# Kernel tuning notes

Hardware: AMD Instinct MI355X
Metric: run time of the kernel (lower is better)

The kernel has to match this reference:

```python
import jax, jax.numpy as jnp
import numpy as np

EPS = 1e-6

def feature_map(x):
    # 'elu' feature map: elu(x) + 1 (positive feature map from Katharopoulos et al.)
    return jax.nn.elu(x) + 1.0

def setup_inputs() -> dict:
    key = jax.random.key(0)
    kq, kk, kv = jax.random.split(key, 3)
    B, L, H, D = 4, 2048, 16, 64
    q = jax.random.normal(kq, (B, L, H, D), dtype=jnp.float32)
    k = jax.random.normal(kk, (B, L, H, D), dtype=jnp.float32)
    v = jax.random.normal(kv, (B, L, H, D), dtype=jnp.float32)
    return {"q": q, "k": k, "v": v}

def reference(q, k, v):
    # q, k, v: [N, L, H, D]  (attention_mask=None -> causal linear attention)
    qf = feature_map(q)
    kf = feature_map(k)
    # normalizer: z[n,l,h] = sum_d qf[n,l,h,d] * cumsum_s<=l kf[n,s,h,d]
    z = jnp.einsum('nlhd,nlhd->nlh', qf, jnp.cumsum(kf, axis=1)) + EPS
    # causal_dot_product via scan over sequence with carry S[n,h,d,m]
    B, L, H, D = q.shape
    M = v.shape[-1]
    qs = jnp.moveaxis(qf, 1, 0)  # [L, N, H, D]
    ks = jnp.moveaxis(kf, 1, 0)
    vs = jnp.moveaxis(v, 1, 0)

    def step(S, qkv):
        ql, kl, vl = qkv                              # [N,H,D], [N,H,D], [N,H,M]
        S = S + jnp.einsum('nhd,nhm->nhdm', kl, vl)   # running sum of k v^T
        out = jnp.einsum('nhd,nhdm->nhm', ql, S)
        return S, out

    S0 = jnp.zeros((B, H, D, M), dtype=q.dtype)
    _, outs = jax.lax.scan(step, S0, (qs, ks, vs))    # outs: [L, N, H, M]
    v_ = jnp.moveaxis(outs, 0, 1)                     # [N, L, H, M]
    return v_ / z[..., None]
```

## Files before the change

kernel.cpp:

```cpp
#include <hip/hip_runtime.h>
#include <cstdint>

#define LL 2048
#define HH 16
#define DD 64
#define LSTR 1024
#define EPSF 1e-6f
#define PAD 72
#define SWZ(row, off) ((row)*PAD + ((off) ^ ((((row)>>3)&7)<<3)))

typedef __bf16 bf16x8 __attribute__((ext_vector_type(8)));
typedef float floatx4 __attribute__((ext_vector_type(4)));
typedef unsigned short ushortx8 __attribute__((ext_vector_type(8)));
typedef unsigned short ushortx4 __attribute__((ext_vector_type(4)));
typedef unsigned short ushortx2 __attribute__((ext_vector_type(2)));

static __device__ __forceinline__ float fmap(float x){ return x > 0.f ? x + 1.f : __expf(x); }
static __device__ __forceinline__ unsigned short f2bf(float f){
    unsigned u = __builtin_bit_cast(unsigned, f);
    u += 0x7fffu + ((u >> 16) & 1u);
    return (unsigned short)(u >> 16);
}
static __device__ __forceinline__ float bf2f(unsigned short s){
    unsigned u = ((unsigned)s) << 16;
    return __builtin_bit_cast(float, u);
}
static __device__ __forceinline__ bf16x8 ldf(const unsigned short* p){
    return __builtin_bit_cast(bf16x8, *(const ushortx8*)p);
}

template<bool MAP>
static __device__ __forceinline__ void st_sd(unsigned short* base, int r, int c, float4 a, float4 b){
    if (MAP) {
        *(ushortx4*)(base + r*PAD + c)     = ushortx4{ f2bf(fmap(a.x)), f2bf(fmap(a.y)), f2bf(fmap(a.z)), f2bf(fmap(a.w)) };
        *(ushortx4*)(base + (r+1)*PAD + c) = ushortx4{ f2bf(fmap(b.x)), f2bf(fmap(b.y)), f2bf(fmap(b.z)), f2bf(fmap(b.w)) };
    } else {
        *(ushortx4*)(base + r*PAD + c)     = ushortx4{ f2bf(a.x), f2bf(a.y), f2bf(a.z), f2bf(a.w) };
        *(ushortx4*)(base + (r+1)*PAD + c) = ushortx4{ f2bf(b.x), f2bf(b.y), f2bf(b.z), f2bf(b.w) };
    }
}
template<bool MAP>
static __device__ __forceinline__ void st_tr(unsigned short* base, int r, int c, float4 a, float4 b){
    float aa[4] = {a.x, a.y, a.z, a.w}, bb[4] = {b.x, b.y, b.z, b.w};
#pragma unroll
    for (int e = 0; e < 4; ++e) {
        float x0 = MAP ? fmap(aa[e]) : aa[e];
        float x1 = MAP ? fmap(bb[e]) : bb[e];
        *(ushortx2*)(base + SWZ(c+e, r)) = ushortx2{ f2bf(x0), f2bf(x1) };
    }
}

__global__ __launch_bounds__(256) void kA(const float* __restrict__ kp, const float* __restrict__ vp,
                                          unsigned short* __restrict__ snap, float* __restrict__ ksnap)
{
    __shared__ __align__(16) unsigned short kft[2][DD*PAD];
    __shared__ __align__(16) unsigned short vtt[2][DD*PAD];
    const int blk = blockIdx.x;
    const int bh = blk >> 3, oct = blk & 7, b = bh >> 4, h = bh & 15;
    const int t = threadIdx.x;
    const int w = t >> 6, lane = t & 63, quad = lane >> 4, lr = lane & 15;
    const int m0 = 16*w;

    floatx4 acc[4];
#pragma unroll
    for (int dt = 0; dt < 4; ++dt) acc[dt] = floatx4{0.f,0.f,0.f,0.f};
    float ksa = 0.f;

    const int64_t gb0 = ((int64_t)(b*LL + oct*256)*HH + h)*DD;
#pragma unroll
    for (int ii = 0; ii < 2; ++ii) {
        int flat = t + 256*ii;
        int l0s = (flat >> 4) * 2, col4 = (flat & 15) << 2;
        const float* gk = kp + gb0 + (int64_t)l0s*LSTR + col4;
        const float* gv = vp + gb0 + (int64_t)l0s*LSTR + col4;
        float4 ka = *(const float4*)gk, kb = *(const float4*)(gk + LSTR);
        float4 va = *(const float4*)gv, vb = *(const float4*)(gv + LSTR);
        st_tr<true >(kft[0], l0s, col4, ka, kb);
        st_tr<false>(vtt[0], l0s, col4, va, vb);
    }
    __syncthreads();

#pragma unroll 1
    for (int sc = 0; sc < 4; ++sc) {
        const int p = sc & 1;
        float4 ka[2], kb[2], va[2], vb[2];
        if (sc < 3) {
            const int64_t gb = gb0 + (int64_t)(sc+1)*DD*LSTR;
#pragma unroll
            for (int ii = 0; ii < 2; ++ii) {
                int flat = t + 256*ii;
                int l0s = (flat >> 4) * 2, col4 = (flat & 15) << 2;
                const float* gk = kp + gb + (int64_t)l0s*LSTR + col4;
                const float* gv = vp + gb + (int64_t)l0s*LSTR + col4;
                ka[ii] = *(const float4*)gk; kb[ii] = *(const float4*)(gk + LSTR);
                va[ii] = *(const float4*)gv; vb[ii] = *(const float4*)(gv + LSTR);
            }
        }
#pragma unroll
        for (int kk = 0; kk < 2; ++kk) {
            bf16x8 a = ldf(vtt[p] + SWZ(m0+lr, kk*32 + quad*8));
#pragma unroll
            for (int dt = 0; dt < 4; ++dt) {
                bf16x8 bbf = ldf(kft[p] + SWZ(dt*16+lr, kk*32 + quad*8));
                acc[dt] = __builtin_amdgcn_mfma_f32_16x16x32_bf16(a, bbf, acc[dt], 0, 0, 0);
            }
        }
        {
            unsigned short* so = snap + ((int64_t)blk*4 + sc)*4096;
#pragma unroll
            for (int dt = 0; dt < 4; ++dt)
#pragma unroll
                for (int r = 0; r < 4; ++r)
                    so[(m0 + quad*4 + r)*DD + dt*16 + lr] = f2bf(acc[dt][r]);
        }
        if (t < DD) {
#pragma unroll
            for (int jj = 0; jj < 8; ++jj) {
                ushortx8 u = *(const ushortx8*)(kft[p] + SWZ(t, jj*8));
#pragma unroll
                for (int e = 0; e < 8; ++e) ksa += bf2f(u[e]);
            }
            ksnap[((int64_t)blk*4 + sc)*DD + t] = ksa;
        }
        if (sc < 3) {
#pragma unroll
            for (int ii = 0; ii < 2; ++ii) {
                int flat = t + 256*ii;
                int l0s = (flat >> 4) * 2, col4 = (flat & 15) << 2;
                st_tr<true >(kft[p^1], l0s, col4, ka[ii], kb[ii]);
                st_tr<false>(vtt[p^1], l0s, col4, va[ii], vb[ii]);
            }
        }
        __syncthreads();
    }
}

__global__ __launch_bounds__(256) void kC(const float* __restrict__ qp, const float* __restrict__ kp,
                                          const float* __restrict__ vp,
                                          const unsigned short* __restrict__ snap,
                                          const float* __restrict__ ksnap,
                                          float* __restrict__ outp)
{
    __shared__ __align__(16) unsigned short qf [DD*PAD];
    __shared__ __align__(16) unsigned short kfx[80*PAD];
    __shared__ __align__(16) unsigned short vtt[DD*PAD];
    __shared__ __align__(16) unsigned short sld[DD*PAD];
    __shared__ float zr[DD];
    const int bid = blockIdx.x;
    const int bh = bid >> 5, c = bid & 31, b = bh >> 4, h = bh & 15;
    const int o = c >> 2, j = c & 3;
    const int t = threadIdx.x;
    const int64_t gbase = ((int64_t)(b*LL + c*DD)*HH + h)*DD;

#pragma unroll
    for (int i = 0; i < 2; ++i) {
        int flat = t + 256*i;
        int l0s = (flat >> 4) * 2, col = (flat & 15) << 2;
        const float* gq = qp + gbase + (int64_t)l0s*LSTR + col;
        const float* gk = kp + gbase + (int64_t)l0s*LSTR + col;
        const float* gv = vp + gbase + (int64_t)l0s*LSTR + col;
        float4 qa = *(const float4*)(gq), qb = *(const float4*)(gq + LSTR);
        float4 ka = *(const float4*)(gk), kb = *(const float4*)(gk + LSTR);
        float4 va = *(const float4*)(gv), vb = *(const float4*)(gv + LSTR);
        st_sd<true >(qf , l0s, col, qa, qb);
        st_sd<true >(kfx, l0s, col, ka, kb);
        st_tr<false>(vtt, l0s, col, va, vb);
    }
    if (t < 135) *(ushortx8*)(kfx + 65*PAD + t*8) = ushortx8{0,0,0,0,0,0,0,0};
    if (t < DD) {
        float s = 0.f;
        for (int op = 0; op < o; ++op) s += ksnap[((int64_t)(bh*8 + op)*4 + 3)*DD + t];
        if (j > 0) s += ksnap[((int64_t)(bh*8 + o)*4 + (j-1))*DD + t];
        kfx[64*PAD + t] = f2bf(s);
    }
    {
        const int m = t >> 2, d0 = (t & 3) << 4;
        float a0[8], a1[8];
#pragma unroll
        for (int e = 0; e < 8; ++e) { a0[e] = 0.f; a1[e] = 0.f; }
        for (int op = 0; op < o; ++op) {
            const unsigned short* sp = snap + ((int64_t)(bh*8 + op)*4 + 3)*4096 + m*DD + d0;
            ushortx8 u0 = *(const ushortx8*)sp, u1 = *(const ushortx8*)(sp + 8);
#pragma unroll
            for (int e = 0; e < 8; ++e) { a0[e] += bf2f(u0[e]); a1[e] += bf2f(u1[e]); }
        }
        if (j > 0) {
            const unsigned short* sp = snap + ((int64_t)(bh*8 + o)*4 + (j-1))*4096 + m*DD + d0;
            ushortx8 u0 = *(const ushortx8*)sp, u1 = *(const ushortx8*)(sp + 8);
#pragma unroll
            for (int e = 0; e < 8; ++e) { a0[e] += bf2f(u0[e]); a1[e] += bf2f(u1[e]); }
        }
        ushortx8 w0, w1;
#pragma unroll
        for (int e = 0; e < 8; ++e) { w0[e] = f2bf(a0[e]); w1[e] = f2bf(a1[e]); }
        *(ushortx8*)(sld + m*PAD + d0)     = w0;
        *(ushortx8*)(sld + m*PAD + d0 + 8) = w1;
    }
    __syncthreads();

    const int w = t >> 6, lane = t & 63, quad = lane >> 4, lr = lane & 15;
    const int l0 = 16*w;
    bf16x8 aq[2];
    aq[0] = ldf(qf + (l0+lr)*PAD + quad*8);
    aq[1] = ldf(qf + (l0+lr)*PAD + 32 + quad*8);
    bf16x8 bs[2][4];
#pragma unroll
    for (int kk = 0; kk < 2; ++kk)
#pragma unroll
        for (int mt = 0; mt < 4; ++mt)
            bs[kk][mt] = ldf(sld + (mt*16+lr)*PAD + kk*32 + quad*8);

    floatx4 sc5[5];
#pragma unroll
    for (int tt = 0; tt < 5; ++tt) sc5[tt] = floatx4{0.f,0.f,0.f,0.f};
#pragma unroll
    for (int kk = 0; kk < 2; ++kk)
#pragma unroll
        for (int tt = 0; tt < 5; ++tt) {
            bf16x8 bb = ldf(kfx + (tt*16+lr)*PAD + kk*32 + quad*8);
            sc5[tt] = __builtin_amdgcn_mfma_f32_16x16x32_bf16(aq[kk], bb, sc5[tt], 0, 0, 0);
        }

    float zp[4] = {0.f,0.f,0.f,0.f};
#pragma unroll
    for (int tt = 0; tt < 4; ++tt)
#pragma unroll
        for (int r = 0; r < 4; ++r) {
            int row = l0 + quad*4 + r;
            int col = tt*16 + lr;
            float val = (col <= row) ? sc5[tt][r] : 0.f;
            zp[r] += val;
            qf[row*PAD + col] = f2bf(val);
        }
#pragma unroll
    for (int r = 0; r < 4; ++r) zp[r] += (lr == 0) ? sc5[4][r] : 0.f;
#pragma unroll
    for (int m = 1; m < 16; m <<= 1)
#pragma unroll
        for (int r = 0; r < 4; ++r) zp[r] += __shfl_xor(zp[r], m, 64);
    if (lr == 0)
#pragma unroll
        for (int r = 0; r < 4; ++r) zr[l0 + quad*4 + r] = 1.f / (zp[r] + EPSF);

    floatx4 oa[4];
#pragma unroll
    for (int mt = 0; mt < 4; ++mt) oa[mt] = floatx4{0.f,0.f,0.f,0.f};
#pragma unroll
    for (int kk = 0; kk < 2; ++kk) {
        bf16x8 a2 = ldf(qf + (l0+lr)*PAD + kk*32 + quad*8);
#pragma unroll
        for (int mt = 0; mt < 4; ++mt) {
            bf16x8 bv = ldf(vtt + SWZ(mt*16+lr, kk*32 + quad*8));
            oa[mt] = __builtin_amdgcn_mfma_f32_16x16x32_bf16(a2, bv, oa[mt], 0, 0, 0);
        }
    }
#pragma unroll
    for (int kk = 0; kk < 2; ++kk)
#pragma unroll
        for (int mt = 0; mt < 4; ++mt)
            oa[mt] = __builtin_amdgcn_mfma_f32_16x16x32_bf16(aq[kk], bs[kk][mt], oa[mt], 0, 0, 0);
#pragma unroll
    for (int r = 0; r < 4; ++r) {
        int row = l0 + quad*4 + r;
        float rz = zr[row];
#pragma unroll
        for (int mt = 0; mt < 4; ++mt)
            outp[gbase + (int64_t)row*LSTR + mt*16 + lr] = oa[mt][r] * rz;
    }
}

extern "C" void kernel_launch(void* const* d_in, const int* in_sizes, int n_in,
                              void* d_out, int out_size, void* d_ws, size_t ws_size,
                              hipStream_t stream) {
    const float* q = (const float*)d_in[0];
    const float* k = (const float*)d_in[1];
    const float* v = (const float*)d_in[2];
    float* out = (float*)d_out;
    unsigned short* snap = (unsigned short*)d_ws;
    float* ksnap = (float*)((char*)d_ws + (size_t)512*4*4096*2);
    kA<<<512,  256, 0, stream>>>(k, v, snap, ksnap);
    kC<<<2048, 256, 0, stream>>>(q, k, v, snap, ksnap, out);
}
```

Baseline: 155.0 us.

## Add prefix-sum kernel, widen chunk kernel, reuse LDS and remap blocks

Adds a middle kernel kB that precomputes, once per octant, the cross-octant prefix sums of the state snapshots and k-sums in fp32. Each kC block then reads one prefix plus at most one intra-octant snapshot, where it previously looped over up to seven snapshots in global memory. Several other changes come with it. kA runs 512 threads so each wave computes half the d-tiles. kC drops the separate state LDS buffer by reusing the v buffer after an extra barrier, sets a min-blocks-per-CU bound of 5, and remaps block IDs. f2bf now uses the compiler's bf16 conversion instead of manual rounding. In exchange there is an extra launch and extra workspace traffic for the fp32 prefixes.

```diff
diff --git a/kernel.cpp b/kernel.cpp
--- a/kernel.cpp
+++ b/kernel.cpp
@@ -17,9 +17,7 @@
 
 static __device__ __forceinline__ float fmap(float x){ return x > 0.f ? x + 1.f : __expf(x); }
 static __device__ __forceinline__ unsigned short f2bf(float f){
-    unsigned u = __builtin_bit_cast(unsigned, f);
-    u += 0x7fffu + ((u >> 16) & 1u);
-    return (unsigned short)(u >> 16);
+    return __builtin_bit_cast(unsigned short, static_cast<__bf16>(f));
 }
 static __device__ __forceinline__ float bf2f(unsigned short s){
     unsigned u = ((unsigned)s) << 16;
@@ -50,7 +48,7 @@
     }
 }
 
-__global__ __launch_bounds__(256) void kA(const float* __restrict__ kp, const float* __restrict__ vp,
+__global__ __launch_bounds__(512) void kA(const float* __restrict__ kp, const float* __restrict__ vp,
                                           unsigned short* __restrict__ snap, float* __restrict__ ksnap)
 {
     __shared__ __align__(16) unsigned short kft[2][DD*PAD];
@@ -59,18 +57,16 @@
     const int bh = blk >> 3, oct = blk & 7, b = bh >> 4, h = bh & 15;
     const int t = threadIdx.x;
     const int w = t >> 6, lane = t & 63, quad = lane >> 4, lr = lane & 15;
-    const int m0 = 16*w;
-
-    floatx4 acc[4];
-#pragma unroll
-    for (int dt = 0; dt < 4; ++dt) acc[dt] = floatx4{0.f,0.f,0.f,0.f};
+    const int m0 = 16*(w & 3), dth = (w >> 2) << 1;
+    const int l0s = (t >> 4) * 2, col4 = (t & 15) << 2;
+
+    floatx4 acc[2];
+    acc[0] = floatx4{0.f,0.f,0.f,0.f};
+    acc[1] = floatx4{0.f,0.f,0.f,0.f};
     float ksa = 0.f;
 
     const int64_t gb0 = ((int64_t)(b*LL + oct*256)*HH + h)*DD;
-#pragma unroll
-    for (int ii = 0; ii < 2; ++ii) {
-        int flat = t + 256*ii;
-        int l0s = (flat >> 4) * 2, col4 = (flat & 15) << 2;
+    {
         const float* gk = kp + gb0 + (int64_t)l0s*LSTR + col4;
         const float* gv = vp + gb0 + (int64_t)l0s*LSTR + col4;
         float4 ka = *(const float4*)gk, kb = *(const float4*)(gk + LSTR);
@@ -83,35 +79,30 @@
 #pragma unroll 1
     for (int sc = 0; sc < 4; ++sc) {
         const int p = sc & 1;
-        float4 ka[2], kb[2], va[2], vb[2];
+        float4 ka, kb, va, vb;
         if (sc < 3) {
             const int64_t gb = gb0 + (int64_t)(sc+1)*DD*LSTR;
-#pragma unroll
-            for (int ii = 0; ii < 2; ++ii) {
-                int flat = t + 256*ii;
-                int l0s = (flat >> 4) * 2, col4 = (flat & 15) << 2;
-                const float* gk = kp + gb + (int64_t)l0s*LSTR + col4;
-                const float* gv = vp + gb + (int64_t)l0s*LSTR + col4;
-                ka[ii] = *(const float4*)gk; kb[ii] = *(const float4*)(gk + LSTR);
-                va[ii] = *(const float4*)gv; vb[ii] = *(const float4*)(gv + LSTR);
-            }
+            const float* gk = kp + gb + (int64_t)l0s*LSTR + col4;
+            const float* gv = vp + gb + (int64_t)l0s*LSTR + col4;
+            ka = *(const float4*)gk; kb = *(const float4*)(gk + LSTR);
+            va = *(const float4*)gv; vb = *(const float4*)(gv + LSTR);
         }
 #pragma unroll
         for (int kk = 0; kk < 2; ++kk) {
             bf16x8 a = ldf(vtt[p] + SWZ(m0+lr, kk*32 + quad*8));
 #pragma unroll
-            for (int dt = 0; dt < 4; ++dt) {
-                bf16x8 bbf = ldf(kft[p] + SWZ(dt*16+lr, kk*32 + quad*8));
-                acc[dt] = __builtin_amdgcn_mfma_f32_16x16x32_bf16(a, bbf, acc[dt], 0, 0, 0);
+            for (int dtl = 0; dtl < 2; ++dtl) {
+                bf16x8 bbf = ldf(kft[p] + SWZ((dth+dtl)*16+lr, kk*32 + quad*8));
+                acc[dtl] = __builtin_amdgcn_mfma_f32_16x16x32_bf16(a, bbf, acc[dtl], 0, 0, 0);
             }
         }
         {
             unsigned short* so = snap + ((int64_t)blk*4 + sc)*4096;
 #pragma unroll
-            for (int dt = 0; dt < 4; ++dt)
+            for (int dtl = 0; dtl < 2; ++dtl)
 #pragma unroll
                 for (int r = 0; r < 4; ++r)
-                    so[(m0 + quad*4 + r)*DD + dt*16 + lr] = f2bf(acc[dt][r]);
+                    so[(m0 + quad*4 + r)*DD + (dth+dtl)*16 + lr] = f2bf(acc[dtl][r]);
         }
         if (t < DD) {
 #pragma unroll
@@ -123,34 +114,88 @@
             ksnap[((int64_t)blk*4 + sc)*DD + t] = ksa;
         }
         if (sc < 3) {
-#pragma unroll
-            for (int ii = 0; ii < 2; ++ii) {
-                int flat = t + 256*ii;
-                int l0s = (flat >> 4) * 2, col4 = (flat & 15) << 2;
-                st_tr<true >(kft[p^1], l0s, col4, ka[ii], kb[ii]);
-                st_tr<false>(vtt[p^1], l0s, col4, va[ii], vb[ii]);
-            }
+            st_tr<true >(kft[p^1], l0s, col4, ka, kb);
+            st_tr<false>(vtt[p^1], l0s, col4, va, vb);
         }
         __syncthreads();
     }
 }
 
-__global__ __launch_bounds__(256) void kC(const float* __restrict__ qp, const float* __restrict__ kp,
-                                          const float* __restrict__ vp,
-                                          const unsigned short* __restrict__ snap,
+__global__ __launch_bounds__(256) void kB(const unsigned short* __restrict__ snap,
                                           const float* __restrict__ ksnap,
-                                          float* __restrict__ outp)
+                                          float* __restrict__ spre, float* __restrict__ kpre)
+{
+    const int blk = blockIdx.x;
+    const int bh = blk >> 3, oct = blk & 7;
+    const int t = threadIdx.x;
+    const int m = t >> 2, d0 = (t & 3) << 4;
+    const unsigned short* sb = snap + (((int64_t)bh*8)*4 + 3)*4096 + m*DD + d0;
+    float acc[16];
+#pragma unroll
+    for (int e = 0; e < 16; ++e) acc[e] = 0.f;
+#pragma unroll
+    for (int half = 0; half < 2; ++half) {
+        ushortx8 u[7];
+#pragma unroll
+        for (int op = 0; op < 7; ++op)
+            if (op < oct) u[op] = *(const ushortx8*)(sb + (int64_t)op*4*4096 + half*8);
+#pragma unroll
+        for (int op = 0; op < 7; ++op)
+            if (op < oct)
+#pragma unroll
+                for (int e = 0; e < 8; ++e) acc[half*8+e] += bf2f(u[op][e]);
+    }
+    float* so = spre + (int64_t)blk*4096 + m*DD + d0;
+#pragma unroll
+    for (int g = 0; g < 4; ++g)
+        *(float4*)(so + 4*g) = float4{acc[4*g], acc[4*g+1], acc[4*g+2], acc[4*g+3]};
+    if (t < DD) {
+        float s = 0.f;
+#pragma unroll
+        for (int op = 0; op < 7; ++op)
+            if (op < oct) s += ksnap[(((int64_t)bh*8 + op)*4 + 3)*DD + t];
+        kpre[(int64_t)blk*DD + t] = s;
+    }
+}
+
+__global__ __launch_bounds__(256, 5) void kC(const float* __restrict__ qp, const float* __restrict__ kp,
+                                             const float* __restrict__ vp,
+                                             const unsigned short* __restrict__ snap,
+                                             const float* __restrict__ ksnap,
+                                             const float* __restrict__ spre,
+                                             const float* __restrict__ kpre,
+                                             float* __restrict__ outp)
 {
     __shared__ __align__(16) unsigned short qf [DD*PAD];
     __shared__ __align__(16) unsigned short kfx[80*PAD];
     __shared__ __align__(16) unsigned short vtt[DD*PAD];
-    __shared__ __align__(16) unsigned short sld[DD*PAD];
     __shared__ float zr[DD];
-    const int bid = blockIdx.x;
+    const int orig = blockIdx.x;
+    const int bid = ((orig & 7) << 8) | (orig >> 3);
     const int bh = bid >> 5, c = bid & 31, b = bh >> 4, h = bh & 15;
     const int o = c >> 2, j = c & 3;
     const int t = threadIdx.x;
     const int64_t gbase = ((int64_t)(b*LL + c*DD)*HH + h)*DD;
+
+    const int sm = t >> 2, sd0 = (t & 3) << 4;
+    ushortx8 sw0, sw1;
+    {
+        const float* pp = spre + ((int64_t)(bh*8 + o))*4096 + sm*DD + sd0;
+        float4 p0 = *(const float4*)(pp);
+        float4 p1 = *(const float4*)(pp + 4);
+        float4 p2 = *(const float4*)(pp + 8);
+        float4 p3 = *(const float4*)(pp + 12);
+        float sa[16] = {p0.x,p0.y,p0.z,p0.w, p1.x,p1.y,p1.z,p1.w,
+                        p2.x,p2.y,p2.z,p2.w, p3.x,p3.y,p3.z,p3.w};
+        if (j > 0) {
+            const unsigned short* sp = snap + (((int64_t)(bh*8 + o))*4 + (j-1))*4096 + sm*DD + sd0;
+            ushortx8 u0 = *(const ushortx8*)sp, u1 = *(const ushortx8*)(sp + 8);
+#pragma unroll
+            for (int e = 0; e < 8; ++e) { sa[e] += bf2f(u0[e]); sa[8+e] += bf2f(u1[e]); }
+        }
+#pragma unroll
+        for (int e = 0; e < 8; ++e) { sw0[e] = f2bf(sa[e]); sw1[e] = f2bf(sa[8+e]); }
+    }
 
 #pragma unroll
     for (int i = 0; i < 2; ++i) {
@@ -168,33 +213,9 @@
     }
     if (t < 135) *(ushortx8*)(kfx + 65*PAD + t*8) = ushortx8{0,0,0,0,0,0,0,0};
     if (t < DD) {
-        float s = 0.f;
-        for (int op = 0; op < o; ++op) s += ksnap[((int64_t)(bh*8 + op)*4 + 3)*DD + t];
-        if (j > 0) s += ksnap[((int64_t)(bh*8 + o)*4 + (j-1))*DD + t];
+        float s = kpre[((int64_t)(bh*8 + o))*DD + t];
+        if (j > 0) s += ksnap[(((int64_t)(bh*8 + o))*4 + (j-1))*DD + t];
         kfx[64*PAD + t] = f2bf(s);
-    }
-    {
-        const int m = t >> 2, d0 = (t & 3) << 4;
-        float a0[8], a1[8];
-#pragma unroll
-        for (int e = 0; e < 8; ++e) { a0[e] = 0.f; a1[e] = 0.f; }
-        for (int op = 0; op < o; ++op) {
-            const unsigned short* sp = snap + ((int64_t)(bh*8 + op)*4 + 3)*4096 + m*DD + d0;
-            ushortx8 u0 = *(const ushortx8*)sp, u1 = *(const ushortx8*)(sp + 8);
-#pragma unroll
-            for (int e = 0; e < 8; ++e) { a0[e] += bf2f(u0[e]); a1[e] += bf2f(u1[e]); }
-        }
-        if (j > 0) {
-            const unsigned short* sp = snap + ((int64_t)(bh*8 + o)*4 + (j-1))*4096 + m*DD + d0;
-            ushortx8 u0 = *(const ushortx8*)sp, u1 = *(const ushortx8*)(sp + 8);
-#pragma unroll
-            for (int e = 0; e < 8; ++e) { a0[e] += bf2f(u0[e]); a1[e] += bf2f(u1[e]); }
-        }
-        ushortx8 w0, w1;
-#pragma unroll
-        for (int e = 0; e < 8; ++e) { w0[e] = f2bf(a0[e]); w1[e] = f2bf(a1[e]); }
-        *(ushortx8*)(sld + m*PAD + d0)     = w0;
-        *(ushortx8*)(sld + m*PAD + d0 + 8) = w1;
     }
     __syncthreads();
 
@@ -203,12 +224,6 @@
     bf16x8 aq[2];
     aq[0] = ldf(qf + (l0+lr)*PAD + quad*8);
     aq[1] = ldf(qf + (l0+lr)*PAD + 32 + quad*8);
-    bf16x8 bs[2][4];
-#pragma unroll
-    for (int kk = 0; kk < 2; ++kk)
-#pragma unroll
-        for (int mt = 0; mt < 4; ++mt)
-            bs[kk][mt] = ldf(sld + (mt*16+lr)*PAD + kk*32 + quad*8);
 
     floatx4 sc5[5];
 #pragma unroll
@@ -254,11 +269,19 @@
             oa[mt] = __builtin_amdgcn_mfma_f32_16x16x32_bf16(a2, bv, oa[mt], 0, 0, 0);
         }
     }
+    __syncthreads();
+
+    *(ushortx8*)(vtt + SWZ(sm, sd0))     = sw0;
+    *(ushortx8*)(vtt + SWZ(sm, sd0 + 8)) = sw1;
+    __syncthreads();
+
 #pragma unroll
     for (int kk = 0; kk < 2; ++kk)
 #pragma unroll
-        for (int mt = 0; mt < 4; ++mt)
-            oa[mt] = __builtin_amdgcn_mfma_f32_16x16x32_bf16(aq[kk], bs[kk][mt], oa[mt], 0, 0, 0);
+        for (int mt = 0; mt < 4; ++mt) {
+            bf16x8 bs = ldf(vtt + SWZ(mt*16+lr, kk*32 + quad*8));
+            oa[mt] = __builtin_amdgcn_mfma_f32_16x16x32_bf16(aq[kk], bs, oa[mt], 0, 0, 0);
+        }
 #pragma unroll
     for (int r = 0; r < 4; ++r) {
         int row = l0 + quad*4 + r;
@@ -276,8 +299,12 @@
     const float* k = (const float*)d_in[1];
     const float* v = (const float*)d_in[2];
     float* out = (float*)d_out;
-    unsigned short* snap = (unsigned short*)d_ws;
-    float* ksnap = (float*)((char*)d_ws + (size_t)512*4*4096*2);
-    kA<<<512,  256, 0, stream>>>(k, v, snap, ksnap);
-    kC<<<2048, 256, 0, stream>>>(q, k, v, snap, ksnap, out);
-}
+    char* ws = (char*)d_ws;
+    unsigned short* snap = (unsigned short*)ws;
+    float* ksnap = (float*)(ws + (size_t)512*4*4096*2);
+    float* spre  = (float*)(ws + (size_t)512*4*4096*2 + 512*4*64*4);
+    float* kpre  = (float*)(ws + (size_t)512*4*4096*2 + 512*4*64*4 + (size_t)512*4096*4);
+    kA<<<512,  512, 0, stream>>>(k, v, snap, ksnap);
+    kB<<<512,  256, 0, stream>>>(snap, ksnap, spre, kpre);
+    kC<<<2048, 256, 0, stream>>>(q, k, v, snap, ksnap, spre, kpre, out);
+}
```

Result: no change. 157.2 us (+1.4%).
